# Performance work log

Hardware: AMD Instinct MI355X
Metric: run time of the kernel (lower is better)

## Reference

```python
import jax, jax.numpy as jnp
import numpy as np

NUM_SEGMENTS = 16
N_MAX = 256
CHUNK = (N_MAX + NUM_SEGMENTS - 1) // NUM_SEGMENTS  # 16
BETA1, BETA2, BETA3 = 0.5, 0.5, 0.4


def _masked_mean(x, mask):
    m = mask.astype(x.dtype)
    s = m.sum()
    return jnp.where(s > 0, (x * m).sum() / jnp.maximum(s, 1.0), jnp.zeros((), x.dtype))


def setup_inputs() -> dict:
    key = jax.random.key(0)
    ks = jax.random.split(key, 10)
    B, S, H, V, Sm, R = 2, 1024, 4096, 32000, 256, 256
    k_hidden = jax.random.normal(ks[0], (B, S, H), dtype=jnp.float32)
    last_hidden = jax.random.normal(ks[1], (B, S, H), dtype=jnp.float32)
    input_ids = jax.random.randint(ks[2], (B, S), 0, V)
    attention_mask = jnp.ones((B, S), dtype=jnp.int32)
    starts = jax.random.randint(ks[3], (B,), 0, 300)
    ends = starts + 200 + jax.random.randint(ks[4], (B,), 0, 100)
    math_lengths = jnp.full((B,), Sm, dtype=jnp.int64 if jax.config.jax_enable_x64 else jnp.int32)
    math_labels = jax.random.randint(ks[5], (B, Sm), 0, V)
    math_attention_mask = jnp.ones((B, Sm), dtype=jnp.int32)
    A_matrices = jax.random.normal(ks[6], (NUM_SEGMENTS, H, R), dtype=jnp.float32) * 0.02
    B_matrices = jax.random.normal(ks[7], (NUM_SEGMENTS, R, H), dtype=jnp.float32) * 0.02
    bias = jnp.zeros((NUM_SEGMENTS, H), dtype=jnp.float32)
    W_lm = jax.random.normal(ks[8], (H, V), dtype=jnp.float32) * 0.02
    return {"k_hidden": k_hidden, "last_hidden": last_hidden, "input_ids": input_ids,
            "attention_mask": attention_mask, "starts": starts, "ends": ends,
            "math_lengths": math_lengths, "math_labels": math_labels,
            "math_attention_mask": math_attention_mask, "A_matrices": A_matrices,
            "B_matrices": B_matrices, "bias": bias, "W_lm": W_lm}


def reference(k_hidden, last_hidden, input_ids, attention_mask, starts, ends,
              math_lengths, math_labels, math_attention_mask,
              A_matrices, B_matrices, bias, W_lm):
    B, S, H = last_hidden.shape
    Sm = math_labels.shape[1]
    n_blk = Sm // CHUNK  # == NUM_SEGMENTS here (N_max == Sm)

    # ---- simple-talk / final-answer CE losses on full logits ----
    logits = jnp.einsum('bsh,hv->bsv', last_hidden, W_lm)  # [B,S,V]
    logp = jax.nn.log_softmax(logits[:, :-1, :], axis=-1)
    labels = input_ids[:, 1:]
    nll = -jnp.take_along_axis(logp, labels[..., None], axis=-1)[..., 0]  # [B,S-1]
    idx = jnp.arange(S - 1)[None, :]
    real_len = attention_mask.sum(axis=1)[:, None]
    mask_simple = (idx >= starts[:, None] - 1) & (idx <= ends[:, None] - 1)
    mask_final = (idx >= ends[:, None]) & (idx < real_len - 1)
    simple_talk_loss = _masked_mean(nll, mask_simple)
    final_answer_loss = _masked_mean(nll, mask_final)

    # ---- math loss: segment-routed LoRA (A @ (B @ h) + bias) then lm_head CE ----
    # mask_hidden selects the contiguous block [starts, starts+math_lengths) per row;
    # with full math_attention_mask this is exactly Sm tokens per row.
    pos = starts[:, None] + jnp.arange(Sm)[None, :]  # [B,Sm]
    math_h = jnp.take_along_axis(k_hidden, pos[:, :, None], axis=1)  # [B,Sm,H]
    # segment_ids are position//CHUNK -> contiguous blocks: grouped GEMM via reshape
    hb = math_h.reshape(B, n_blk, CHUNK, H)
    inter = jnp.einsum('bsch,srh->bscr', hb, B_matrices)      # B_seg @ h
    trans = jnp.einsum('bscr,shr->bsch', inter, A_matrices)   # A_seg @ inter
    trans = trans + bias[None, :, None, :]
    t = trans.reshape(B * Sm, H)
    mlogits = t @ W_lm                                        # [B*Sm, V]
    mlogp = jax.nn.log_softmax(mlogits, axis=-1)
    tgt = math_labels.reshape(-1)
    mnll = -jnp.take_along_axis(mlogp, tgt[:, None], axis=-1)[:, 0]  # [B*Sm]
    math_loss = mnll.mean()
    # per-segment mean losses (diagnostic, no-grad in original)
    A_losses = jax.lax.stop_gradient(mnll.reshape(B, n_blk, CHUNK).mean(axis=(0, 2)))

    total_loss = BETA1 * math_loss + BETA2 * simple_talk_loss + BETA3 * final_answer_loss
    return total_loss, math_loss, simple_talk_loss, final_answer_loss, A_losses
```

## Files before the change

kernel.cpp:

```cpp
#include <hip/hip_runtime.h>

#define NSEG 16
#define CH   16
#define Bb   2
#define Ss   1024
#define Hh   4096
#define Vv   32000
#define SMm  256
#define Rr   256

#define M_MAIN 2046
#define M_MATH 512
#define M_REAL 2558
#define M_PAD  2560

#define BM 256
#define BN 128
#define BK 128
#define NT_M (M_PAD/BM)
#define NT_N (Vv/BN)
#define KT   (Hh/BK)
#define NWG  (NT_M*NT_N)
#define NQG  (Hh/16)

#define HC   8
#define HCL  (Hh/HC)
#define PART_STRIDE (Bb*NSEG*CH*Rr)

typedef __attribute__((ext_vector_type(4))) float    floatx4;
typedef __attribute__((ext_vector_type(4))) int      intx4;
typedef __attribute__((ext_vector_type(8))) int      intx8;

#define ASCALE 16.f
#define WSCALE 256.f
#define DESCALE (1.f/(16.f*256.f))

template<bool W>
__device__ __forceinline__ int cvtpk(float a, float b, int old) {
  return __builtin_amdgcn_cvt_pk_fp8_f32(a, b, old, W);
}

__device__ __forceinline__ void gload_lds16(const void* g, void* l) {
  __builtin_amdgcn_global_load_lds((const __attribute__((address_space(1))) void*)g,
                                   (__attribute__((address_space(3))) void*)l, 16, 0, 0);
}

__global__ __launch_bounds__(256) void k_convA(const float* __restrict__ lh, intx4* __restrict__ Aq) {
  int row = blockIdx.x * 256 + threadIdx.x;
  int qgg = blockIdx.y;
  if (row >= M_MAIN) return;
  int b = row / (Ss - 1), s = row % (Ss - 1);
  const floatx4* src = (const floatx4*)(lh + ((size_t)(b * Ss + s)) * Hh + qgg * 16);
  floatx4 f0 = src[0], f1 = src[1], f2 = src[2], f3 = src[3];
  int p0 = cvtpk<false>(f0[0]*ASCALE, f0[1]*ASCALE, 0); p0 = cvtpk<true>(f0[2]*ASCALE, f0[3]*ASCALE, p0);
  int p1 = cvtpk<false>(f1[0]*ASCALE, f1[1]*ASCALE, 0); p1 = cvtpk<true>(f1[2]*ASCALE, f1[3]*ASCALE, p1);
  int p2 = cvtpk<false>(f2[0]*ASCALE, f2[1]*ASCALE, 0); p2 = cvtpk<true>(f2[2]*ASCALE, f2[3]*ASCALE, p2);
  int p3 = cvtpk<false>(f3[0]*ASCALE, f3[1]*ASCALE, 0); p3 = cvtpk<true>(f3[2]*ASCALE, f3[3]*ASCALE, p3);
  Aq[(size_t)qgg * M_PAD + row] = (intx4){p0, p1, p2, p3};
}

__global__ __launch_bounds__(256) void k_convW(const float* __restrict__ W, intx4* __restrict__ Wf) {
  int v = blockIdx.x * 256 + threadIdx.x;
  int qgg = blockIdx.y;
  const float* base = W + (size_t)(qgg * 16) * Vv + v;
  int p[4];
  #pragma unroll
  for (int q = 0; q < 4; ++q) {
    float e0 = base[(size_t)(4*q+0) * Vv] * WSCALE;
    float e1 = base[(size_t)(4*q+1) * Vv] * WSCALE;
    float e2 = base[(size_t)(4*q+2) * Vv] * WSCALE;
    float e3 = base[(size_t)(4*q+3) * Vv] * WSCALE;
    int pp = cvtpk<false>(e0, e1, 0);
    p[q] = cvtpk<true>(e2, e3, pp);
  }
  Wf[(size_t)qgg * Vv + v] = (intx4){p[0], p[1], p[2], p[3]};
}

__global__ __launch_bounds__(256) void k_inter2(const float* __restrict__ kh, const float* __restrict__ Bm,
                                                const int* __restrict__ starts, float* __restrict__ part) {
  int bid = blockIdx.x;
  int b = bid >> 7, seg = (bid >> 3) & 15, hc = bid & 7;
  int tid = threadIdx.x;
  __shared__ float sX[CH][HCL];
  int st = starts[b];
  for (int i = tid; i < CH * (HCL / 4); i += 256) {
    int c = i / (HCL / 4), k4 = i % (HCL / 4);
    int pos = st + seg * CH + c;
    ((floatx4*)&sX[c][0])[k4] = *(const floatx4*)(kh + ((size_t)(b * Ss + pos)) * Hh + hc * HCL + 4 * k4);
  }
  __syncthreads();
  const floatx4* w = (const floatx4*)(Bm + ((size_t)(seg * Rr + tid)) * Hh + hc * HCL);
  float acc[CH];
  #pragma unroll
  for (int c = 0; c < CH; ++c) acc[c] = 0.f;
  for (int i = 0; i < HCL / 4; ++i) {
    floatx4 w4 = w[i];
    #pragma unroll
    for (int c = 0; c < CH; ++c)
      acc[c] += w4[0]*sX[c][4*i] + w4[1]*sX[c][4*i+1] + w4[2]*sX[c][4*i+2] + w4[3]*sX[c][4*i+3];
  }
  float* dst = part + (size_t)hc * PART_STRIDE + ((size_t)(b * NSEG + seg)) * CH * Rr;
  #pragma unroll
  for (int c = 0; c < CH; ++c) dst[c * Rr + tid] = acc[c];
}

__global__ __launch_bounds__(256) void k_trans(const float* __restrict__ part, const float* __restrict__ Am,
                                               const float* __restrict__ bias, intx4* __restrict__ Aq) {
  int bid = blockIdx.x;
  int b = bid >> 7, seg = (bid >> 3) & 15, ht = bid & 7;
  int tid = threadIdx.x;
  __shared__ float sI[CH][Rr];
  const float* ib = part + ((size_t)(b * NSEG + seg)) * CH * Rr;
  for (int i = tid; i < CH * Rr / 4; i += 256) {
    floatx4 s = ((const floatx4*)ib)[i];
    #pragma unroll
    for (int hc = 1; hc < HC; ++hc)
      s += ((const floatx4*)(ib + (size_t)hc * PART_STRIDE))[i];
    ((floatx4*)&sI[0][0])[i] = s;
  }
  __syncthreads();
  unsigned char* Ab = (unsigned char*)Aq;
  for (int hh = 0; hh < 2; ++hh) {
    int h = (ht << 9) + (tid << 1) + hh;
    const floatx4* ar = (const floatx4*)(Am + ((size_t)(seg * Hh + h)) * Rr);
    float acc[CH];
    #pragma unroll
    for (int c = 0; c < CH; ++c) acc[c] = 0.f;
    for (int i = 0; i < Rr / 4; ++i) {
      floatx4 a4 = ar[i];
      #pragma unroll
      for (int c = 0; c < CH; ++c)
        acc[c] += a4[0]*sI[c][i*4] + a4[1]*sI[c][i*4+1] + a4[2]*sI[c][i*4+2] + a4[3]*sI[c][i*4+3];
    }
    float bv = bias[seg * Hh + h];
    #pragma unroll
    for (int c = 0; c < CH; ++c) {
      int row = M_MAIN + b * SMm + seg * CH + c;
      int pk = cvtpk<false>((acc[c] + bv) * ASCALE, 0.f, 0);
      Ab[(((size_t)(h >> 4)) * M_PAD + row) * 16 + (h & 15)] = (unsigned char)(pk & 0xFF);
    }
  }
}

__global__ __launch_bounds__(256) void k_labels(const int* __restrict__ input_ids, const int* __restrict__ mlab,
                                                int* __restrict__ labels, float* __restrict__ llog,
                                                intx4* __restrict__ Aq) {
  int t = blockIdx.x * 256 + threadIdx.x;
  if (t < M_PAD) {
    int lab;
    if (t < M_MAIN)      { int b = t / (Ss - 1), s = t % (Ss - 1); lab = input_ids[b * Ss + s + 1]; }
    else if (t < M_REAL) { lab = mlab[t - M_MAIN]; }
    else                 { lab = 0x7fffffff; }
    labels[t] = lab;
    llog[t] = 0.f;
  }
  if (t < 2 * NQG) {
    int qgg = t >> 1, row = M_REAL + (t & 1);
    Aq[(size_t)qgg * M_PAD + row] = (intx4){0, 0, 0, 0};
  }
}

__global__ __launch_bounds__(512, 2) void k_gemm_mx2(const intx4* __restrict__ Aq, const intx4* __restrict__ Wf,
                                                     const int* __restrict__ labels, float* __restrict__ pmax,
                                                     float* __restrict__ psum, float* __restrict__ llog) {
  __shared__ intx4 As[3][8][BM];
  __shared__ intx4 Bs[3][8][BN];
  __shared__ float redM[BM * 2];
  __shared__ float redS[BM * 2];

  int bid = blockIdx.x;
  int mt = bid % NT_M, nt = bid / NT_M;
  int m0 = mt * BM, n0 = nt * BN;
  int tid = threadIdx.x;
  int lane = tid & 63;
  int wid = tid >> 6;
  int wr = wid >> 1, wc = wid & 1;
  int l15 = lane & 15, l4 = lane >> 4;

  floatx4 acc[4][4];
  #pragma unroll
  for (int m = 0; m < 4; ++m)
    #pragma unroll
    for (int n = 0; n < 4; ++n) acc[m][n] = (floatx4){0.f, 0.f, 0.f, 0.f};

#define STAGE(tt, bb) do {                                                              \
    const intx4* ab_ = Aq + (size_t)(tt) * 8 * M_PAD;                                   \
    _Pragma("unroll")                                                                   \
    for (int it_ = 0; it_ < 4; ++it_) {                                                 \
      int s_ = it_ * 512 + tid;                                                         \
      gload_lds16(ab_ + ((size_t)(s_ >> 8) * M_PAD + m0 + (s_ & 255)),                  \
                  (void*)(&As[bb][0][0] + s_));                                         \
    }                                                                                   \
    const intx4* wb_ = Wf + (size_t)(tt) * 8 * Vv;                                      \
    _Pragma("unroll")                                                                   \
    for (int it_ = 0; it_ < 2; ++it_) {                                                 \
      int s_ = it_ * 512 + tid;                                                         \
      gload_lds16(wb_ + ((size_t)(s_ >> 7) * Vv + n0 + (s_ & 127)),                     \
                  (void*)(&Bs[bb][0][0] + s_));                                         \
    }                                                                                   \
  } while (0)

  STAGE(0, 0);
  STAGE(1, 1);
  int cur = 0;

  for (int kt = 0; kt < KT; ++kt) {
    if (kt < KT - 1) {
      asm volatile("s_waitcnt vmcnt(6)" ::: "memory");
    } else {
      asm volatile("s_waitcnt vmcnt(0)" ::: "memory");
    }
    __builtin_amdgcn_s_barrier();
    __builtin_amdgcn_sched_barrier(0);

    intx8 a[4], b[4];
    #pragma unroll
    for (int m = 0; m < 4; ++m) {
      int row = wr * 64 + m * 16 + l15;
      intx4 lo = As[cur][2 * l4][row];
      intx4 hi = As[cur][2 * l4 + 1][row];
      a[m] = __builtin_shufflevector(lo, hi, 0, 1, 2, 3, 4, 5, 6, 7);
    }
    #pragma unroll
    for (int n = 0; n < 4; ++n) {
      int col = wc * 64 + n * 16 + l15;
      intx4 lo = Bs[cur][2 * l4][col];
      intx4 hi = Bs[cur][2 * l4 + 1][col];
      b[n] = __builtin_shufflevector(lo, hi, 0, 1, 2, 3, 4, 5, 6, 7);
    }

    if (kt + 2 < KT) STAGE(kt + 2, (cur + 2) % 3);

    __builtin_amdgcn_s_setprio(1);
    #pragma unroll
    for (int m = 0; m < 4; ++m)
      #pragma unroll
      for (int n = 0; n < 4; ++n)
        acc[m][n] = __builtin_amdgcn_mfma_scale_f32_16x16x128_f8f6f4(
            a[m], b[n], acc[m][n], 0, 0, 0, 0x7F7F7F7F, 0, 0x7F7F7F7F);
    __builtin_amdgcn_s_setprio(0);

    cur = (cur + 1) % 3;
  }
#undef STAGE

  #pragma unroll
  for (int m = 0; m < 4; ++m)
    #pragma unroll
    for (int n = 0; n < 4; ++n) acc[m][n] *= DESCALE;

  __syncthreads();

  #pragma unroll
  for (int m = 0; m < 4; ++m) {
    #pragma unroll
    for (int r = 0; r < 4; ++r) {
      int grow = m0 + wr * 64 + m * 16 + l4 * 4 + r;
      int lab = (grow < M_REAL) ? labels[grow] : -1;
      #pragma unroll
      for (int n = 0; n < 4; ++n) {
        int gcol = n0 + wc * 64 + n * 16 + l15;
        if (lab == gcol) llog[grow] = acc[m][n][r];
      }
    }
  }
  float rm[4][4];
  #pragma unroll
  for (int m = 0; m < 4; ++m)
    #pragma unroll
    for (int r = 0; r < 4; ++r) {
      float v = fmaxf(fmaxf(acc[m][0][r], acc[m][1][r]), fmaxf(acc[m][2][r], acc[m][3][r]));
      v = fmaxf(v, __shfl_xor(v, 1));
      v = fmaxf(v, __shfl_xor(v, 2));
      v = fmaxf(v, __shfl_xor(v, 4));
      v = fmaxf(v, __shfl_xor(v, 8));
      rm[m][r] = v;
    }
  if (l15 == 0) {
    #pragma unroll
    for (int m = 0; m < 4; ++m)
      #pragma unroll
      for (int r = 0; r < 4; ++r)
        redM[(wr * 64 + m * 16 + l4 * 4 + r) * 2 + wc] = rm[m][r];
  }
  __syncthreads();
  #pragma unroll
  for (int m = 0; m < 4; ++m)
    #pragma unroll
    for (int r = 0; r < 4; ++r) {
      int row = wr * 64 + m * 16 + l4 * 4 + r;
      float tmx = fmaxf(redM[row * 2], redM[row * 2 + 1]);
      float s = 0.f;
      #pragma unroll
      for (int n = 0; n < 4; ++n) s += __expf(acc[m][n][r] - tmx);
      s += __shfl_xor(s, 1);
      s += __shfl_xor(s, 2);
      s += __shfl_xor(s, 4);
      s += __shfl_xor(s, 8);
      rm[m][r] = s;
    }
  if (l15 == 0) {
    #pragma unroll
    for (int m = 0; m < 4; ++m)
      #pragma unroll
      for (int r = 0; r < 4; ++r)
        redS[(wr * 64 + m * 16 + l4 * 4 + r) * 2 + wc] = rm[m][r];
  }
  __syncthreads();
  if (tid < BM) {
    int grow = m0 + tid;
    if (grow < M_REAL) {
      float tmx = fmaxf(redM[tid * 2], redM[tid * 2 + 1]);
      float s = redS[tid * 2] + redS[tid * 2 + 1];
      pmax[(size_t)grow * NT_N + nt] = tmx;
      psum[(size_t)grow * NT_N + nt] = s;
    }
  }
}

__global__ __launch_bounds__(256) void k_fin(const float* __restrict__ pmax, const float* __restrict__ psum,
                                             const float* __restrict__ llog, float* __restrict__ nll) {
  int row = blockIdx.x * 4 + (threadIdx.x >> 6);
  int lane = threadIdx.x & 63;
  if (row >= M_REAL) return;
  float m = -3.4e38f;
  for (int t = lane; t < NT_N; t += 64) m = fmaxf(m, pmax[(size_t)row * NT_N + t]);
  #pragma unroll
  for (int d = 1; d < 64; d <<= 1) m = fmaxf(m, __shfl_xor(m, d));
  float s = 0.f;
  for (int t = lane; t < NT_N; t += 64)
    s += psum[(size_t)row * NT_N + t] * __expf(pmax[(size_t)row * NT_N + t] - m);
  #pragma unroll
  for (int d = 1; d < 64; d <<= 1) s += __shfl_xor(s, d);
  if (lane == 0) nll[row] = logf(s) + m - llog[row];
}

__global__ __launch_bounds__(256) void k_loss(const float* __restrict__ nll, const int* __restrict__ starts,
                                              const int* __restrict__ ends, const int* __restrict__ attn,
                                              float* __restrict__ out) {
  __shared__ float rA[256], rB[256], rC[256], rD[256];
  __shared__ float smath[M_MATH];
  __shared__ float rl[2];
  int tid = threadIdx.x;
  for (int b = 0; b < 2; ++b) {
    float p = 0.f;
    for (int i = tid; i < Ss; i += 256) p += (float)attn[b * Ss + i];
    rA[tid] = p;
    __syncthreads();
    if (tid == 0) { float t = 0.f; for (int i = 0; i < 256; ++i) t += rA[i]; rl[b] = t; }
    __syncthreads();
  }
  float ss = 0.f, sc = 0.f, fs = 0.f, fc = 0.f;
  int st0 = starts[0], st1 = starts[1], en0 = ends[0], en1 = ends[1];
  for (int r = tid; r < M_MAIN; r += 256) {
    int b = r / (Ss - 1), idx = r % (Ss - 1);
    int st = b ? st1 : st0, en = b ? en1 : en0;
    int rlen = (int)rl[b];
    float v = nll[r];
    if (idx >= st - 1 && idx <= en - 1) { ss += v; sc += 1.f; }
    if (idx >= en && idx < rlen - 1)    { fs += v; fc += 1.f; }
  }
  rA[tid] = ss; rB[tid] = sc; rC[tid] = fs; rD[tid] = fc;
  for (int j = tid; j < M_MATH; j += 256) smath[j] = nll[M_MAIN + j];
  __syncthreads();
  if (tid == 0) {
    float SS = 0.f, SC = 0.f, FS = 0.f, FC = 0.f;
    for (int i = 0; i < 256; ++i) { SS += rA[i]; SC += rB[i]; FS += rC[i]; FC += rD[i]; }
    float MS = 0.f;
    for (int j = 0; j < M_MATH; ++j) MS += smath[j];
    float math_loss = MS / (float)M_MATH;
    float simple = (SC > 0.f) ? SS / fmaxf(SC, 1.f) : 0.f;
    float fin    = (FC > 0.f) ? FS / fmaxf(FC, 1.f) : 0.f;
    out[0] = 0.5f * math_loss + 0.5f * simple + 0.4f * fin;
    out[1] = math_loss;
    out[2] = simple;
    out[3] = fin;
    for (int seg = 0; seg < NSEG; ++seg) {
      float a = 0.f;
      for (int b = 0; b < 2; ++b)
        for (int c = 0; c < CH; ++c) a += smath[b * SMm + seg * CH + c];
      out[4 + seg] = a / 32.f;
    }
  }
}

extern "C" void kernel_launch(void* const* d_in, const int* in_sizes, int n_in,
                              void* d_out, int out_size, void* d_ws, size_t ws_size,
                              hipStream_t stream) {
  const float* k_hidden    = (const float*)d_in[0];
  const float* last_hidden = (const float*)d_in[1];
  const int*   input_ids   = (const int*)d_in[2];
  const int*   attn        = (const int*)d_in[3];
  const int*   starts      = (const int*)d_in[4];
  const int*   ends        = (const int*)d_in[5];
  const int*   math_labels = (const int*)d_in[7];
  const float* A_matrices  = (const float*)d_in[9];
  const float* B_matrices  = (const float*)d_in[10];
  const float* bias        = (const float*)d_in[11];
  const float* W_lm        = (const float*)d_in[12];
  float* out = (float*)d_out;

  char* ws = (char*)d_ws;
  size_t off = 0;
  intx4* Wf   = (intx4*)ws;                 off += (size_t)NQG * Vv * 16;
  intx4* Aq   = (intx4*)(ws + off);         off += (size_t)NQG * M_PAD * 16;
  float* part = (float*)(ws + off);         off += (size_t)HC * PART_STRIDE * 4;
  int*   labels = (int*)(ws + off);         off += (size_t)M_PAD * 4;
  float* llog   = (float*)(ws + off);       off += (size_t)M_PAD * 4;
  float* pmax   = (float*)(ws + off);       off += (size_t)M_PAD * NT_N * 4;
  float* psum   = (float*)(ws + off);       off += (size_t)M_PAD * NT_N * 4;
  float* nll    = (float*)(ws + off);       off += (size_t)M_PAD * 4;

  {
    dim3 ga((M_MAIN + 255) / 256, NQG);
    k_convA<<<ga, 256, 0, stream>>>(last_hidden, Aq);
  }
  k_inter2<<<Bb * NSEG * HC, 256, 0, stream>>>(k_hidden, B_matrices, starts, part);
  k_trans<<<Bb * NSEG * 8, 256, 0, stream>>>(part, A_matrices, bias, Aq);
  k_labels<<<(M_PAD + 255) / 256, 256, 0, stream>>>(input_ids, math_labels, labels, llog, Aq);
  {
    dim3 gw(Vv / 256, NQG);
    k_convW<<<gw, 256, 0, stream>>>(W_lm, Wf);
  }
  k_gemm_mx2<<<NWG, 512, 0, stream>>>(Aq, Wf, labels, pmax, psum, llog);
  k_fin<<<(M_REAL + 3) / 4, 256, 0, stream>>>(pmax, psum, llog, nll);
  k_loss<<<1, 256, 0, stream>>>(nll, starts, ends, attn, out);
}
```

Before: 600.1 us.

## Halve GEMM M-tile, switch to double-buffered LDS with pointer-stepped staging

Shrinks the MX-fp8 LM-head GEMM tile from 256x128 to 128x128, so each wave computes 2x4 MFMA fragments instead of 4x4. The LDS pipeline drops from triple to double buffering, with a second barrier before refilling the consumed buffer. Staging now uses precomputed pointers that advance each k-step. The aim is higher occupancy (launch bounds 4) and more workgroups to spread over CUs, at the cost of less reuse of W per A tile, twice the W traffic and an extra barrier per iteration.

```diff
diff --git a/kernel.cpp b/kernel.cpp
--- a/kernel.cpp
+++ b/kernel.cpp
@@ -14,7 +14,7 @@
 #define M_REAL 2558
 #define M_PAD  2560
 
-#define BM 256
+#define BM 128
 #define BN 128
 #define BK 128
 #define NT_M (M_PAD/BM)
@@ -160,11 +160,11 @@
   }
 }
 
-__global__ __launch_bounds__(512, 2) void k_gemm_mx2(const intx4* __restrict__ Aq, const intx4* __restrict__ Wf,
+__global__ __launch_bounds__(512, 4) void k_gemm_mx3(const intx4* __restrict__ Aq, const intx4* __restrict__ Wf,
                                                      const int* __restrict__ labels, float* __restrict__ pmax,
                                                      float* __restrict__ psum, float* __restrict__ llog) {
-  __shared__ intx4 As[3][8][BM];
-  __shared__ intx4 Bs[3][8][BN];
+  __shared__ intx4 As[2][8][BM];
+  __shared__ intx4 Bs[2][8][BN];
   __shared__ float redM[BM * 2];
   __shared__ float redS[BM * 2];
 
@@ -177,85 +177,77 @@
   int wr = wid >> 1, wc = wid & 1;
   int l15 = lane & 15, l4 = lane >> 4;
 
-  floatx4 acc[4][4];
-  #pragma unroll
-  for (int m = 0; m < 4; ++m)
+  floatx4 acc[2][4];
+  #pragma unroll
+  for (int m = 0; m < 2; ++m)
     #pragma unroll
     for (int n = 0; n < 4; ++n) acc[m][n] = (floatx4){0.f, 0.f, 0.f, 0.f};
 
-#define STAGE(tt, bb) do {                                                              \
-    const intx4* ab_ = Aq + (size_t)(tt) * 8 * M_PAD;                                   \
-    _Pragma("unroll")                                                                   \
-    for (int it_ = 0; it_ < 4; ++it_) {                                                 \
-      int s_ = it_ * 512 + tid;                                                         \
-      gload_lds16(ab_ + ((size_t)(s_ >> 8) * M_PAD + m0 + (s_ & 255)),                  \
-                  (void*)(&As[bb][0][0] + s_));                                         \
-    }                                                                                   \
-    const intx4* wb_ = Wf + (size_t)(tt) * 8 * Vv;                                      \
-    _Pragma("unroll")                                                                   \
-    for (int it_ = 0; it_ < 2; ++it_) {                                                 \
-      int s_ = it_ * 512 + tid;                                                         \
-      gload_lds16(wb_ + ((size_t)(s_ >> 7) * Vv + n0 + (s_ & 127)),                     \
-                  (void*)(&Bs[bb][0][0] + s_));                                         \
-    }                                                                                   \
+  int tq = tid >> 7, tr = tid & 127;
+  const intx4* pA = Aq + (size_t)tq * M_PAD + m0 + tr;
+  const intx4* pB = Wf + (size_t)tq * Vv + n0 + tr;
+
+#define STAGE(bb) do {                                        \
+    gload_lds16(pA,                 &As[bb][tq][tr]);         \
+    gload_lds16(pA + 4 * (size_t)M_PAD, &As[bb][tq + 4][tr]); \
+    gload_lds16(pB,                 &Bs[bb][tq][tr]);         \
+    gload_lds16(pB + 4 * (size_t)Vv,    &Bs[bb][tq + 4][tr]); \
+    pA += 8 * (size_t)M_PAD; pB += 8 * (size_t)Vv;            \
   } while (0)
 
-  STAGE(0, 0);
-  STAGE(1, 1);
-  int cur = 0;
+  STAGE(0);
+  STAGE(1);
 
   for (int kt = 0; kt < KT; ++kt) {
+    int cb = kt & 1;
     if (kt < KT - 1) {
-      asm volatile("s_waitcnt vmcnt(6)" ::: "memory");
+      asm volatile("s_waitcnt vmcnt(4)" ::: "memory");
     } else {
       asm volatile("s_waitcnt vmcnt(0)" ::: "memory");
     }
     __builtin_amdgcn_s_barrier();
     __builtin_amdgcn_sched_barrier(0);
 
-    intx8 a[4], b[4];
-    #pragma unroll
-    for (int m = 0; m < 4; ++m) {
-      int row = wr * 64 + m * 16 + l15;
-      intx4 lo = As[cur][2 * l4][row];
-      intx4 hi = As[cur][2 * l4 + 1][row];
-      a[m] = __builtin_shufflevector(lo, hi, 0, 1, 2, 3, 4, 5, 6, 7);
+    union frag { intx8 v; struct { intx4 lo, hi; } h; };
+    frag a[2], b[4];
+    #pragma unroll
+    for (int m = 0; m < 2; ++m) {
+      int row = wr * 32 + m * 16 + l15;
+      a[m].h.lo = As[cb][2 * l4][row];
+      a[m].h.hi = As[cb][2 * l4 + 1][row];
     }
     #pragma unroll
     for (int n = 0; n < 4; ++n) {
       int col = wc * 64 + n * 16 + l15;
-      intx4 lo = Bs[cur][2 * l4][col];
-      intx4 hi = Bs[cur][2 * l4 + 1][col];
-      b[n] = __builtin_shufflevector(lo, hi, 0, 1, 2, 3, 4, 5, 6, 7);
-    }
-
-    if (kt + 2 < KT) STAGE(kt + 2, (cur + 2) % 3);
+      b[n].h.lo = Bs[cb][2 * l4][col];
+      b[n].h.hi = Bs[cb][2 * l4 + 1][col];
+    }
 
     __builtin_amdgcn_s_setprio(1);
     #pragma unroll
-    for (int m = 0; m < 4; ++m)
+    for (int m = 0; m < 2; ++m)
       #pragma unroll
       for (int n = 0; n < 4; ++n)
         acc[m][n] = __builtin_amdgcn_mfma_scale_f32_16x16x128_f8f6f4(
-            a[m], b[n], acc[m][n], 0, 0, 0, 0x7F7F7F7F, 0, 0x7F7F7F7F);
+            a[m].v, b[n].v, acc[m][n], 0, 0, 0, 0x7F7F7F7F, 0, 0x7F7F7F7F);
     __builtin_amdgcn_s_setprio(0);
 
-    cur = (cur + 1) % 3;
+    __builtin_amdgcn_s_barrier();
+    __builtin_amdgcn_sched_barrier(0);
+    if (kt + 2 < KT) STAGE(cb);
   }
 #undef STAGE
 
   #pragma unroll
-  for (int m = 0; m < 4; ++m)
+  for (int m = 0; m < 2; ++m)
     #pragma unroll
     for (int n = 0; n < 4; ++n) acc[m][n] *= DESCALE;
 
-  __syncthreads();
-
-  #pragma unroll
-  for (int m = 0; m < 4; ++m) {
+  #pragma unroll
+  for (int m = 0; m < 2; ++m) {
     #pragma unroll
     for (int r = 0; r < 4; ++r) {
-      int grow = m0 + wr * 64 + m * 16 + l4 * 4 + r;
+      int grow = m0 + wr * 32 + m * 16 + l4 * 4 + r;
       int lab = (grow < M_REAL) ? labels[grow] : -1;
       #pragma unroll
       for (int n = 0; n < 4; ++n) {
@@ -264,9 +256,9 @@
       }
     }
   }
-  float rm[4][4];
-  #pragma unroll
-  for (int m = 0; m < 4; ++m)
+  float rm[2][4];
+  #pragma unroll
+  for (int m = 0; m < 2; ++m)
     #pragma unroll
     for (int r = 0; r < 4; ++r) {
       float v = fmaxf(fmaxf(acc[m][0][r], acc[m][1][r]), fmaxf(acc[m][2][r], acc[m][3][r]));
@@ -276,19 +268,20 @@
       v = fmaxf(v, __shfl_xor(v, 8));
       rm[m][r] = v;
     }
+  __syncthreads();
   if (l15 == 0) {
     #pragma unroll
-    for (int m = 0; m < 4; ++m)
+    for (int m = 0; m < 2; ++m)
       #pragma unroll
       for (int r = 0; r < 4; ++r)
-        redM[(wr * 64 + m * 16 + l4 * 4 + r) * 2 + wc] = rm[m][r];
-  }
-  __syncthreads();
-  #pragma unroll
-  for (int m = 0; m < 4; ++m)
+        redM[(wr * 32 + m * 16 + l4 * 4 + r) * 2 + wc] = rm[m][r];
+  }
+  __syncthreads();
+  #pragma unroll
+  for (int m = 0; m < 2; ++m)
     #pragma unroll
     for (int r = 0; r < 4; ++r) {
-      int row = wr * 64 + m * 16 + l4 * 4 + r;
+      int row = wr * 32 + m * 16 + l4 * 4 + r;
       float tmx = fmaxf(redM[row * 2], redM[row * 2 + 1]);
       float s = 0.f;
       #pragma unroll
@@ -301,10 +294,10 @@
     }
   if (l15 == 0) {
     #pragma unroll
-    for (int m = 0; m < 4; ++m)
+    for (int m = 0; m < 2; ++m)
       #pragma unroll
       for (int r = 0; r < 4; ++r)
-        redS[(wr * 64 + m * 16 + l4 * 4 + r) * 2 + wc] = rm[m][r];
+        redS[(wr * 32 + m * 16 + l4 * 4 + r) * 2 + wc] = rm[m][r];
   }
   __syncthreads();
   if (tid < BM) {
@@ -422,7 +415,7 @@
     dim3 gw(Vv / 256, NQG);
     k_convW<<<gw, 256, 0, stream>>>(W_lm, Wf);
   }
-  k_gemm_mx2<<<NWG, 512, 0, stream>>>(Aq, Wf, labels, pmax, psum, llog);
+  k_gemm_mx3<<<NWG, 512, 0, stream>>>(Aq, Wf, labels, pmax, psum, llog);
   k_fin<<<(M_REAL + 3) / 4, 256, 0, stream>>>(pmax, psum, llog, nll);
   k_loss<<<1, 256, 0, stream>>>(nll, starts, ends, attn, out);
 }
```

New measurement: 742.5 us. 1.24x slower.
